# Kernel optimization log

Hardware: AMD Instinct MI355X
Metric: run time of the kernel (lower is better)

The kernel has to match this reference:

```python
import math
import jax, jax.numpy as jnp
import numpy as np

SLOPE = 25.0  # surrogate_slope
BETA1 = math.exp(-1.0 / 5.0)   # tau_mso_ms=5
BETA2 = math.exp(-1.0 / 10.0)  # tau_ic_ms=10
THR1 = 1.0
THR2 = 1.0

@jax.custom_vjp
def spike(x):
    return (x > 0).astype(x.dtype)

def _spike_fwd(x):
    return spike(x), x

def _spike_bwd(x, g):
    # fast_sigmoid surrogate: d/dx heaviside ~ 1/(slope*|x|+1)^2
    return (g / (SLOPE * jnp.abs(x) + 1.0) ** 2,)

spike.defvjp(_spike_fwd, _spike_bwd)


def setup_inputs() -> dict:
    key = jax.random.key(0)
    ks = jax.random.split(key, 7)
    T, B, F, H1, H2 = 1000, 256, 64, 256, 256
    spikes = (jax.random.uniform(ks[0], (T, B, F)) < 0.2).astype(jnp.float32)
    s1 = 1.0 / math.sqrt(F)
    s2 = 1.0 / math.sqrt(H1)
    s3 = 1.0 / math.sqrt(H2)
    return {
        "spikes": spikes,
        "W1": jax.random.uniform(ks[1], (H1, F), minval=-s1, maxval=s1),
        "b1": jax.random.uniform(ks[2], (H1,), minval=-s1, maxval=s1),
        "W2": jax.random.uniform(ks[3], (H2, H1), minval=-s2, maxval=s2),
        "b2": jax.random.uniform(ks[4], (H2,), minval=-s2, maxval=s2),
        "Wr": jax.random.uniform(ks[5], (2, H2), minval=-s3, maxval=s3),
        "br": jax.random.uniform(ks[6], (2,), minval=-s3, maxval=s3),
    }


def _snn_forward(spikes, W1, b1, W2, b2, Wr, br):
    T, B, _ = spikes.shape
    H1, H2 = W1.shape[0], W2.shape[0]
    mem1_0 = jnp.zeros((B, H1), spikes.dtype)
    mem2_0 = jnp.zeros((B, H2), spikes.dtype)
    mem2_sum_0 = jnp.zeros((B, H2), spikes.dtype)

    def step(carry, x_t):
        mem1, mem2, mem2_sum = carry
        # layer 1: Linear -> Leaky (reset from previous mem, detached)
        cur1 = x_t @ W1.T + b1
        reset1 = jax.lax.stop_gradient((mem1 > THR1).astype(mem1.dtype))
        mem1 = BETA1 * mem1 + cur1 - reset1 * THR1
        spk1 = spike(mem1 - THR1)
        # layer 2
        cur2 = spk1 @ W2.T + b2
        reset2 = jax.lax.stop_gradient((mem2 > THR2).astype(mem2.dtype))
        mem2 = BETA2 * mem2 + cur2 - reset2 * THR2
        spk2 = spike(mem2 - THR2)
        mem2_sum = mem2_sum + mem2
        return (mem1, mem2, mem2_sum), (spk1.mean(), spk2.mean())

    (_, _, mem2_sum), (spk1_means, spk2_means) = jax.lax.scan(
        step, (mem1_0, mem2_0, mem2_sum_0), spikes)
    mem2_avg = mem2_sum / jnp.asarray(T, spikes.dtype)
    out = mem2_avg @ Wr.T + br  # [B, 2]
    stats = jnp.stack([spk1_means.mean(), spk2_means.mean()])
    return out, stats


def reference(spikes, W1, b1, W2, b2, Wr, br):
    return _snn_forward(spikes, W1, b1, W2, b2, Wr, br)
```

## Files before the change

kernel.cpp:

```cpp
#include <hip/hip_runtime.h>
#include <stdint.h>

#define TSTEPS 1000
#define NB 256
#define NF 64
#define NH 256
#define CHUNK 8
#define NCH 125

__global__ void snn_prep(const float* __restrict__ W2, float* __restrict__ W2T,
                         unsigned int* __restrict__ counts) {
    int idx = blockIdx.x * 256 + threadIdx.x;
    W2T[idx] = W2[(idx & 255) * 256 + (idx >> 8)];
    if (idx < 2) counts[idx] = 0u;
}

#define LDQ(i, wa, wb, wc, wd) \
    { float4 t_ = W1v[i]; wa = t_.x; wb = t_.y; wc = t_.z; wd = t_.w; }
#define PIN4(a, b, c, d) asm("" : "+v"(a), "+v"(b), "+v"(c), "+v"(d));

#define MAQ(acc, fb, wa, wb, wc, wd) \
    acc += ((xm >> (fb)) & 1ull) ? (wa) : 0.f; \
    acc += ((xm >> ((fb) + 1)) & 1ull) ? (wb) : 0.f; \
    acc += ((xm >> ((fb) + 2)) & 1ull) ? (wc) : 0.f; \
    acc += ((xm >> ((fb) + 3)) & 1ull) ? (wd) : 0.f;

#define PSTEP(pb, tt, xv) do {                                                \
    unsigned long long xm = __ballot((xv) > 0.f);                             \
    float a0 = 0.f, a1 = 0.f, a2 = 0.f, a3 = 0.f;                             \
    MAQ(a0, 0,  w00, w01, w02, w03) MAQ(a0, 4,  w04, w05, w06, w07)           \
    MAQ(a0, 8,  w08, w09, w10, w11) MAQ(a0, 12, w12, w13, w14, w15)           \
    MAQ(a1, 16, w16, w17, w18, w19) MAQ(a1, 20, w20, w21, w22, w23)           \
    MAQ(a1, 24, w24, w25, w26, w27) MAQ(a1, 28, w28, w29, w30, w31)           \
    MAQ(a2, 32, w32, w33, w34, w35) MAQ(a2, 36, w36, w37, w38, w39)           \
    MAQ(a2, 40, w40, w41, w42, w43) MAQ(a2, 44, w44, w45, w46, w47)           \
    MAQ(a3, 48, w48, w49, w50, w51) MAQ(a3, 52, w52, w53, w54, w55)           \
    MAQ(a3, 56, w56, w57, w58, w59) MAQ(a3, 60, w60, w61, w62, w63)           \
    float cur1 = b1h + ((a0 + a1) + (a2 + a3));                               \
    float reset1 = (mem1 > 1.f) ? 1.f : 0.f;                                  \
    mem1 = 0.8187307530779818f * mem1 + cur1 - reset1;   \
    bool s1 = (mem1 - 1.f) > 0.f;                                             \
    cnt1 += (int)s1;                                                          \
    unsigned long long sm = __ballot(s1);                                     \
    if (lane == 0) scnt8[pb][(tt) * 4 + wv] = (unsigned char)__popcll(sm);    \
    if (s1) {                                                                 \
        int rank = __popcll(sm & ((1ull << lane) - 1ull));                    \
        slist[pb][tt][(wv << 6) + rank] = (unsigned char)h;                   \
    }                                                                         \
} while (0)

#define CSTEP(cb, tt) do {                                                    \
    unsigned int cwv = *(const unsigned int*)&scnt8[cb][(tt) * 4];            \
    unsigned int u0 = *(const unsigned int*)&slist[cb][tt][0];                \
    unsigned int u1 = *(const unsigned int*)&slist[cb][tt][64];               \
    unsigned int u2 = *(const unsigned int*)&slist[cb][tt][128];              \
    unsigned int u3 = *(const unsigned int*)&slist[cb][tt][192];              \
    int c0 = (int)(cwv & 255u),        c1 = (int)((cwv >> 8) & 255u);         \
    int c2 = (int)((cwv >> 16) & 255u), c3 = (int)((cwv >> 24) & 255u);       \
    float q0 = 0.f, q1 = 0.f, q2 = 0.f, q3 = 0.f;                             \
    _Pragma("unroll")                                                         \
    for (int i = 0; i < 4; ++i) {                                             \
        float v0 = W2Th[(int)((u0 >> (8 * i)) & 255u) << 8];                  \
        float v1 = W2Th[(int)((u1 >> (8 * i)) & 255u) << 8];                  \
        float v2 = W2Th[(int)((u2 >> (8 * i)) & 255u) << 8];                  \
        float v3 = W2Th[(int)((u3 >> (8 * i)) & 255u) << 8];                  \
        q0 += (i < c0) ? v0 : 0.f;                                            \
        q1 += (i < c1) ? v1 : 0.f;                                            \
        q2 += (i < c2) ? v2 : 0.f;                                            \
        q3 += (i < c3) ? v3 : 0.f;                                            \
    }                                                                         \
    int nmax = max(max(c0, c1), max(c2, c3));                                 \
    if (nmax > 4) {        \
        const unsigned char* sl = &slist[cb][tt][0];                          \
        for (int i = 4; i < nmax; ++i) {                                      \
            if (i < c0) q0 += W2Th[(int)sl[i] << 8];                          \
            if (i < c1) q1 += W2Th[(int)sl[64 + i] << 8];                     \
            if (i < c2) q2 += W2Th[(int)sl[128 + i] << 8];                    \
            if (i < c3) q3 += W2Th[(int)sl[192 + i] << 8];                    \
        }                                                                     \
    }                                                                         \
    float cur2 = b2h + ((q0 + q1) + (q2 + q3));                               \
    float reset2 = (mem2 > 1.f) ? 1.f : 0.f;                                  \
    mem2 = 0.9048374180359595f * mem2 + cur2 - reset2;  \
    bool s2 = (mem2 - 1.f) > 0.f;                                             \
    cnt2 += (int)s2;                                                          \
    mem2s += mem2;                                                            \
} while (0)

__attribute__((amdgpu_flat_work_group_size(512, 512), amdgpu_waves_per_eu(2, 2)))
__global__ void snn_main(const float* __restrict__ spikes,
                         const float* __restrict__ W1,
                         const float* __restrict__ b1,
                         const float* __restrict__ W2T,
                         const float* __restrict__ b2,
                         const float* __restrict__ Wr,
                         const float* __restrict__ br,
                         float* __restrict__ out,
                         unsigned int* __restrict__ counts) {
    const int b = blockIdx.x;
    const int tid = threadIdx.x;
    const int lane = tid & 63;
    const int wv = tid >> 6;
    const bool producer = (wv < 4);
    const int h = tid & 255;

    __shared__ unsigned char slist[2][CHUNK][256];
    __shared__ unsigned char scnt8[2][CHUNK * 4];
    __shared__ float rp0[4], rp1[4];
    __shared__ int rc1[4], rc2[4];

    const size_t xstride = (size_t)NB * NF;
    const float* xbase = spikes + (size_t)b * NF + lane;
    const float* W2Th = W2T + h;

    float w00 = 0.f, w01 = 0.f, w02 = 0.f, w03 = 0.f, w04 = 0.f, w05 = 0.f;
    float w06 = 0.f, w07 = 0.f, w08 = 0.f, w09 = 0.f, w10 = 0.f, w11 = 0.f;
    float w12 = 0.f, w13 = 0.f, w14 = 0.f, w15 = 0.f, w16 = 0.f, w17 = 0.f;
    float w18 = 0.f, w19 = 0.f, w20 = 0.f, w21 = 0.f, w22 = 0.f, w23 = 0.f;
    float w24 = 0.f, w25 = 0.f, w26 = 0.f, w27 = 0.f, w28 = 0.f, w29 = 0.f;
    float w30 = 0.f, w31 = 0.f, w32 = 0.f, w33 = 0.f, w34 = 0.f, w35 = 0.f;
    float w36 = 0.f, w37 = 0.f, w38 = 0.f, w39 = 0.f, w40 = 0.f, w41 = 0.f;
    float w42 = 0.f, w43 = 0.f, w44 = 0.f, w45 = 0.f, w46 = 0.f, w47 = 0.f;
    float w48 = 0.f, w49 = 0.f, w50 = 0.f, w51 = 0.f, w52 = 0.f, w53 = 0.f;
    float w54 = 0.f, w55 = 0.f, w56 = 0.f, w57 = 0.f, w58 = 0.f, w59 = 0.f;
    float w60 = 0.f, w61 = 0.f, w62 = 0.f, w63 = 0.f;

    float mem1 = 0.f, mem2 = 0.f, mem2s = 0.f;
    int cnt1 = 0, cnt2 = 0;
    float b1h = 0.f, b2h = 0.f;
    float xq0 = 0.f, xq1 = 0.f, xq2 = 0.f, xq3 = 0.f;
    float xq4 = 0.f, xq5 = 0.f, xq6 = 0.f, xq7 = 0.f;

    if (producer) {
        const float4* W1v = (const float4*)(W1 + h * NF);
        LDQ(0,  w00, w01, w02, w03) LDQ(1,  w04, w05, w06, w07)
        LDQ(2,  w08, w09, w10, w11) LDQ(3,  w12, w13, w14, w15)
        LDQ(4,  w16, w17, w18, w19) LDQ(5,  w20, w21, w22, w23)
        LDQ(6,  w24, w25, w26, w27) LDQ(7,  w28, w29, w30, w31)
        LDQ(8,  w32, w33, w34, w35) LDQ(9,  w36, w37, w38, w39)
        LDQ(10, w40, w41, w42, w43) LDQ(11, w44, w45, w46, w47)
        LDQ(12, w48, w49, w50, w51) LDQ(13, w52, w53, w54, w55)
        LDQ(14, w56, w57, w58, w59) LDQ(15, w60, w61, w62, w63)
        PIN4(w00, w01, w02, w03) PIN4(w04, w05, w06, w07)
        PIN4(w08, w09, w10, w11) PIN4(w12, w13, w14, w15)
        PIN4(w16, w17, w18, w19) PIN4(w20, w21, w22, w23)
        PIN4(w24, w25, w26, w27) PIN4(w28, w29, w30, w31)
        PIN4(w32, w33, w34, w35) PIN4(w36, w37, w38, w39)
        PIN4(w40, w41, w42, w43) PIN4(w44, w45, w46, w47)
        PIN4(w48, w49, w50, w51) PIN4(w52, w53, w54, w55)
        PIN4(w56, w57, w58, w59) PIN4(w60, w61, w62, w63)
        b1h = b1[h];
        xq0 = xbase[0];
        xq1 = xbase[xstride];
        xq2 = xbase[2 * xstride];
        xq3 = xbase[3 * xstride];
        xq4 = xbase[4 * xstride];
        xq5 = xbase[5 * xstride];
        xq6 = xbase[6 * xstride];
        xq7 = xbase[7 * xstride];
    } else {
        b2h = b2[h];
    }

    for (int c = 0; c < NCH; ++c) {
        if (producer) {
            const int pb = c & 1;
            PSTEP(pb, 0, xq0); PSTEP(pb, 1, xq1);
            PSTEP(pb, 2, xq2); PSTEP(pb, 3, xq3);
            PSTEP(pb, 4, xq4); PSTEP(pb, 5, xq5);
            PSTEP(pb, 6, xq6); PSTEP(pb, 7, xq7);
            int cn = (c + 1 < NCH) ? c + 1 : 0;
            const float* xb = xbase + (size_t)cn * CHUNK * xstride;
            xq0 = xb[0];
            xq1 = xb[xstride];
            xq2 = xb[2 * xstride];
            xq3 = xb[3 * xstride];
            xq4 = xb[4 * xstride];
            xq5 = xb[5 * xstride];
            xq6 = xb[6 * xstride];
            xq7 = xb[7 * xstride];
        } else if (c > 0) {
            const int cb = (c - 1) & 1;
            CSTEP(cb, 0); CSTEP(cb, 1); CSTEP(cb, 2); CSTEP(cb, 3);
            CSTEP(cb, 4); CSTEP(cb, 5); CSTEP(cb, 6); CSTEP(cb, 7);
        }
        __syncthreads();
    }
    if (!producer) {
        const int cb = (NCH - 1) & 1;
        CSTEP(cb, 0); CSTEP(cb, 1); CSTEP(cb, 2); CSTEP(cb, 3);
        CSTEP(cb, 4); CSTEP(cb, 5); CSTEP(cb, 6); CSTEP(cb, 7);
    }

    if (producer) {
        int rcs1 = cnt1;
        for (int off = 32; off > 0; off >>= 1) rcs1 += __shfl_down(rcs1, off);
        if (lane == 0) rc1[wv] = rcs1;
    } else {
        float v = mem2s / 1000.0f;
        float p0 = v * Wr[h];
        float p1 = v * Wr[NH + h];
        int rcs2 = cnt2;
        for (int off = 32; off > 0; off >>= 1) {
            p0 += __shfl_down(p0, off);
            p1 += __shfl_down(p1, off);
            rcs2 += __shfl_down(rcs2, off);
        }
        if (lane == 0) { rp0[wv - 4] = p0; rp1[wv - 4] = p1; rc2[wv - 4] = rcs2; }
    }
    __syncthreads();
    if (tid == 0) {
        out[2 * b]     = ((rp0[0] + rp0[1]) + (rp0[2] + rp0[3])) + br[0];
        out[2 * b + 1] = ((rp1[0] + rp1[1]) + (rp1[2] + rp1[3])) + br[1];
        atomicAdd(&counts[0], (unsigned)(rc1[0] + rc1[1] + rc1[2] + rc1[3]));
        atomicAdd(&counts[1], (unsigned)(rc2[0] + rc2[1] + rc2[2] + rc2[3]));
    }
}

__global__ void snn_finalize(const unsigned int* __restrict__ counts,
                             float* __restrict__ out) {
    if (threadIdx.x < 2)
        out[512 + threadIdx.x] = (float)counts[threadIdx.x] / 65536000.0f;
}

extern "C" void kernel_launch(void* const* d_in, const int* in_sizes, int n_in,
                              void* d_out, int out_size, void* d_ws, size_t ws_size,
                              hipStream_t stream) {
    const float* spikes = (const float*)d_in[0];
    const float* W1     = (const float*)d_in[1];
    const float* b1     = (const float*)d_in[2];
    const float* W2     = (const float*)d_in[3];
    const float* b2     = (const float*)d_in[4];
    const float* Wr     = (const float*)d_in[5];
    const float* br     = (const float*)d_in[6];
    float* out = (float*)d_out;

    float* W2T = (float*)d_ws;
    unsigned int* counts = (unsigned int*)((char*)d_ws + (size_t)NH * NH * sizeof(float));

    snn_prep<<<256, 256, 0, stream>>>(W2, W2T, counts);
    snn_main<<<256, 512, 0, stream>>>(spikes, W1, b1, W2T, b2, Wr, br, out, counts);
    snn_finalize<<<1, 64, 0, stream>>>(counts, out);
}
```

Baseline: 727.5 us.

## Stage W1 transposed in LDS and sum only active input spikes

The producer waves no longer keep all 64 W1 weights pinned in registers and evaluate 64 predicated adds per timestep. W1 is now copied transposed into shared memory, and each step walks only the set bits of the input ballot in four 16-feature groups, reading one LDS weight per active spike. With about 20% input firing this cuts the arithmetic per step and frees many VGPRs. In exchange it adds LDS reads, a loop whose trip count depends on data (the largest group decides how long the wave runs), a 64KB LDS array that may limit occupancy, and an extra block-wide sync.

```diff
diff --git a/kernel.cpp b/kernel.cpp
--- a/kernel.cpp
+++ b/kernel.cpp
@@ -15,27 +15,19 @@
     if (idx < 2) counts[idx] = 0u;
 }
 
-#define LDQ(i, wa, wb, wc, wd) \
-    { float4 t_ = W1v[i]; wa = t_.x; wb = t_.y; wc = t_.z; wd = t_.w; }
-#define PIN4(a, b, c, d) asm("" : "+v"(a), "+v"(b), "+v"(c), "+v"(d));
-
-#define MAQ(acc, fb, wa, wb, wc, wd) \
-    acc += ((xm >> (fb)) & 1ull) ? (wa) : 0.f; \
-    acc += ((xm >> ((fb) + 1)) & 1ull) ? (wb) : 0.f; \
-    acc += ((xm >> ((fb) + 2)) & 1ull) ? (wc) : 0.f; \
-    acc += ((xm >> ((fb) + 3)) & 1ull) ? (wd) : 0.f;
-
 #define PSTEP(pb, tt, xv) do {                                                \
     unsigned long long xm = __ballot((xv) > 0.f);                             \
+    unsigned xm0 = (unsigned)(xm & 0xFFFFull);                                \
+    unsigned xm1 = (unsigned)((xm >> 16) & 0xFFFFull);                        \
+    unsigned xm2 = (unsigned)((xm >> 32) & 0xFFFFull);                        \
+    unsigned xm3 = (unsigned)((xm >> 48) & 0xFFFFull);                        \
     float a0 = 0.f, a1 = 0.f, a2 = 0.f, a3 = 0.f;                             \
-    MAQ(a0, 0,  w00, w01, w02, w03) MAQ(a0, 4,  w04, w05, w06, w07)           \
-    MAQ(a0, 8,  w08, w09, w10, w11) MAQ(a0, 12, w12, w13, w14, w15)           \
-    MAQ(a1, 16, w16, w17, w18, w19) MAQ(a1, 20, w20, w21, w22, w23)           \
-    MAQ(a1, 24, w24, w25, w26, w27) MAQ(a1, 28, w28, w29, w30, w31)           \
-    MAQ(a2, 32, w32, w33, w34, w35) MAQ(a2, 36, w36, w37, w38, w39)           \
-    MAQ(a2, 40, w40, w41, w42, w43) MAQ(a2, 44, w44, w45, w46, w47)           \
-    MAQ(a3, 48, w48, w49, w50, w51) MAQ(a3, 52, w52, w53, w54, w55)           \
-    MAQ(a3, 56, w56, w57, w58, w59) MAQ(a3, 60, w60, w61, w62, w63)           \
+    while (xm0 | xm1 | xm2 | xm3) {                                           \
+        if (xm0) { int f = __builtin_ctz(xm0); xm0 &= xm0 - 1; a0 += W1T[f][h]; }      \
+        if (xm1) { int f = __builtin_ctz(xm1); xm1 &= xm1 - 1; a1 += W1T[f + 16][h]; } \
+        if (xm2) { int f = __builtin_ctz(xm2); xm2 &= xm2 - 1; a2 += W1T[f + 32][h]; } \
+        if (xm3) { int f = __builtin_ctz(xm3); xm3 &= xm3 - 1; a3 += W1T[f + 48][h]; } \
+    }                                                                         \
     float cur1 = b1h + ((a0 + a1) + (a2 + a3));                               \
     float reset1 = (mem1 > 1.f) ? 1.f : 0.f;                                  \
     mem1 = 0.8187307530779818f * mem1 + cur1 - reset1;   \
@@ -87,7 +79,7 @@
     mem2s += mem2;                                                            \
 } while (0)
 
-__attribute__((amdgpu_flat_work_group_size(512, 512), amdgpu_waves_per_eu(2, 2)))
+__launch_bounds__(512, 2)
 __global__ void snn_main(const float* __restrict__ spikes,
                          const float* __restrict__ W1,
                          const float* __restrict__ b1,
@@ -104,6 +96,7 @@
     const bool producer = (wv < 4);
     const int h = tid & 255;
 
+    __shared__ float W1T[NF][NH + 1];
     __shared__ unsigned char slist[2][CHUNK][256];
     __shared__ unsigned char scnt8[2][CHUNK * 4];
     __shared__ float rp0[4], rp1[4];
@@ -113,17 +106,9 @@
     const float* xbase = spikes + (size_t)b * NF + lane;
     const float* W2Th = W2T + h;
 
-    float w00 = 0.f, w01 = 0.f, w02 = 0.f, w03 = 0.f, w04 = 0.f, w05 = 0.f;
-    float w06 = 0.f, w07 = 0.f, w08 = 0.f, w09 = 0.f, w10 = 0.f, w11 = 0.f;
-    float w12 = 0.f, w13 = 0.f, w14 = 0.f, w15 = 0.f, w16 = 0.f, w17 = 0.f;
-    float w18 = 0.f, w19 = 0.f, w20 = 0.f, w21 = 0.f, w22 = 0.f, w23 = 0.f;
-    float w24 = 0.f, w25 = 0.f, w26 = 0.f, w27 = 0.f, w28 = 0.f, w29 = 0.f;
-    float w30 = 0.f, w31 = 0.f, w32 = 0.f, w33 = 0.f, w34 = 0.f, w35 = 0.f;
-    float w36 = 0.f, w37 = 0.f, w38 = 0.f, w39 = 0.f, w40 = 0.f, w41 = 0.f;
-    float w42 = 0.f, w43 = 0.f, w44 = 0.f, w45 = 0.f, w46 = 0.f, w47 = 0.f;
-    float w48 = 0.f, w49 = 0.f, w50 = 0.f, w51 = 0.f, w52 = 0.f, w53 = 0.f;
-    float w54 = 0.f, w55 = 0.f, w56 = 0.f, w57 = 0.f, w58 = 0.f, w59 = 0.f;
-    float w60 = 0.f, w61 = 0.f, w62 = 0.f, w63 = 0.f;
+    for (int i = tid; i < NH * NF; i += 512) {
+        W1T[i & 63][i >> 6] = W1[i];
+    }
 
     float mem1 = 0.f, mem2 = 0.f, mem2s = 0.f;
     int cnt1 = 0, cnt2 = 0;
@@ -132,23 +117,6 @@
     float xq4 = 0.f, xq5 = 0.f, xq6 = 0.f, xq7 = 0.f;
 
     if (producer) {
-        const float4* W1v = (const float4*)(W1 + h * NF);
-        LDQ(0,  w00, w01, w02, w03) LDQ(1,  w04, w05, w06, w07)
-        LDQ(2,  w08, w09, w10, w11) LDQ(3,  w12, w13, w14, w15)
-        LDQ(4,  w16, w17, w18, w19) LDQ(5,  w20, w21, w22, w23)
-        LDQ(6,  w24, w25, w26, w27) LDQ(7,  w28, w29, w30, w31)
-        LDQ(8,  w32, w33, w34, w35) LDQ(9,  w36, w37, w38, w39)
-        LDQ(10, w40, w41, w42, w43) LDQ(11, w44, w45, w46, w47)
-        LDQ(12, w48, w49, w50, w51) LDQ(13, w52, w53, w54, w55)
-        LDQ(14, w56, w57, w58, w59) LDQ(15, w60, w61, w62, w63)
-        PIN4(w00, w01, w02, w03) PIN4(w04, w05, w06, w07)
-        PIN4(w08, w09, w10, w11) PIN4(w12, w13, w14, w15)
-        PIN4(w16, w17, w18, w19) PIN4(w20, w21, w22, w23)
-        PIN4(w24, w25, w26, w27) PIN4(w28, w29, w30, w31)
-        PIN4(w32, w33, w34, w35) PIN4(w36, w37, w38, w39)
-        PIN4(w40, w41, w42, w43) PIN4(w44, w45, w46, w47)
-        PIN4(w48, w49, w50, w51) PIN4(w52, w53, w54, w55)
-        PIN4(w56, w57, w58, w59) PIN4(w60, w61, w62, w63)
         b1h = b1[h];
         xq0 = xbase[0];
         xq1 = xbase[xstride];
@@ -161,6 +129,7 @@
     } else {
         b2h = b2[h];
     }
+    __syncthreads();
 
     for (int c = 0; c < NCH; ++c) {
         if (producer) {
```

New measurement: 955.5 us. 31.3% more time.
